# Kernel optimization log

Hardware: AMD Instinct MI355X
Metric: run time of the kernel (lower is better)

Reference implementation:

```python
import jax, jax.numpy as jnp
import numpy as np


def setup_inputs() -> dict:
    key = jax.random.key(0)
    k1, k2, k3 = jax.random.split(key, 3)
    B, H, S, D = 4, 16, 2048, 64
    return {
        "key": jax.random.normal(k1, (B, H, S, D), dtype=jnp.float32),
        "value": jax.random.normal(k2, (B, H, S, D), dtype=jnp.float32),
        "query": jax.random.normal(k3, (B, H, S, D), dtype=jnp.float32),
        # causal mask: True = attend, matches torch masked_fill_(~mask, -inf)
        "mask": jnp.tril(jnp.ones((S, S), dtype=jnp.bool_)),
    }


def reference(key, value, query, mask):
    # scores[b,h,q,k] = query . key^T  (mask applied before scaling as in the
    # source; -inf survives the divide so this equals standard masked attn)
    d = key.shape[-1]
    scores = jnp.einsum("bhqd,bhkd->bhqk", query, key)
    scores = jnp.where(mask, scores, -jnp.inf)
    scores = scores / jnp.sqrt(jnp.asarray(d, dtype=scores.dtype))
    attn = jax.nn.softmax(scores, axis=-1)
    # dropout omitted for a deterministic reference (eval mode)
    return jnp.einsum("bhqk,bhkd->bhqd", attn, value)
```

## Files before the change

### kernel.cpp

```cpp
#include <hip/hip_runtime.h>
#include <hip/hip_bf16.h>

typedef __attribute__((ext_vector_type(4))) float  f32x4;
typedef __attribute__((ext_vector_type(16))) float f32x16;
typedef __attribute__((ext_vector_type(8))) short  bf16x8v;
typedef __attribute__((ext_vector_type(4))) short  bf16x4v;

__device__ __forceinline__ unsigned short f2bf(float x) {
  __bf16 h = (__bf16)x;
  return __builtin_bit_cast(unsigned short, h);
}
__device__ __forceinline__ unsigned pk2(float lo, float hi2) {
  return (unsigned)f2bf(lo) | ((unsigned)f2bf(hi2) << 16);
}

constexpr int S  = 2048;
constexpr int D  = 64;
constexpr int BQ = 256;
constexpr int BK = 64;
#define KSCALE 0.18033688011112042f
#define DTHR   40.0f

__global__ __launch_bounds__(512, 4) void attn_fwd(
    const float* __restrict__ Kg, const float* __restrict__ Vg,
    const float* __restrict__ Qg, float* __restrict__ Og) {
  __shared__ unsigned short Kl[BK * D];
  __shared__ unsigned short Vt[D * BK];

  const int tid  = threadIdx.x;
  const int lane = tid & 63;
  const int w    = tid >> 6;
  const int l31  = lane & 31;
  const int hi   = lane >> 5;

  const int idx = (int)blockIdx.x;
  const int bh  = idx >> 3;
  const int qb  = (idx < 256) ? (7 - (idx & 7)) : (idx & 7);
  const int q0  = qb * BQ;

  const size_t base = (size_t)bh * S * D;
  const float* Kp = Kg + base;
  const float* Vp = Vg + base;
  const float* Qp = Qg + base;
  float*       Op = Og + base;

  const int qrow = q0 + w * 32 + l31;

  const int  st  = tid & 255;
  const bool isK = tid < 256;
  const int  krow = st >> 2, kcol0 = 16 * (st & 3);
  const int  kby0 = kcol0 * 2, kswz = (krow & 7) << 4;
  const int  vk0 = 4 * (st >> 4), vd0 = 4 * (st & 15);

  f32x4 pf0, pf1, pf2, pf3;

  auto LOAD = [&](int kt) {
    if (isK) {
      const float* p = Kp + (size_t)(kt * BK + krow) * D + kcol0;
      pf0 = *(const f32x4*)(p);      pf1 = *(const f32x4*)(p + 4);
      pf2 = *(const f32x4*)(p + 8);  pf3 = *(const f32x4*)(p + 12);
    } else {
      const float* p = Vp + (size_t)(kt * BK + vk0) * D + vd0;
      pf0 = *(const f32x4*)(p);          pf1 = *(const f32x4*)(p + D);
      pf2 = *(const f32x4*)(p + 2 * D);  pf3 = *(const f32x4*)(p + 3 * D);
    }
  };
  auto WRITE = [&]() {
    if (isK) {
      bf16x8v c0, c1;
      c0[0] = f2bf(pf0[0]); c0[1] = f2bf(pf0[1]); c0[2] = f2bf(pf0[2]); c0[3] = f2bf(pf0[3]);
      c0[4] = f2bf(pf1[0]); c0[5] = f2bf(pf1[1]); c0[6] = f2bf(pf1[2]); c0[7] = f2bf(pf1[3]);
      c1[0] = f2bf(pf2[0]); c1[1] = f2bf(pf2[1]); c1[2] = f2bf(pf2[2]); c1[3] = f2bf(pf2[3]);
      c1[4] = f2bf(pf3[0]); c1[5] = f2bf(pf3[1]); c1[6] = f2bf(pf3[2]); c1[7] = f2bf(pf3[3]);
      *(bf16x8v*)((char*)Kl + krow * 128 + ((kby0)      ^ kswz)) = c0;
      *(bf16x8v*)((char*)Kl + krow * 128 + ((kby0 + 16) ^ kswz)) = c1;
    } else {
#pragma unroll
      for (int j = 0; j < 4; ++j) {
        const int d = vd0 + j;
        bf16x4v tb;
        tb[0] = f2bf(pf0[j]); tb[1] = f2bf(pf1[j]);
        tb[2] = f2bf(pf2[j]); tb[3] = f2bf(pf3[j]);
        *(bf16x4v*)((char*)Vt + d * 128 + ((vk0 * 2) ^ ((d & 7) << 4))) = tb;
      }
    }
  };

  bf16x8v qf[4];
#pragma unroll
  for (int c = 0; c < 4; ++c) {
    const float* src = Qp + (size_t)qrow * D + c * 16 + hi * 8;
    f32x4 a = *(const f32x4*)src;
    f32x4 b = *(const f32x4*)(src + 4);
    bf16x8v f;
    f[0] = f2bf(a[0]); f[1] = f2bf(a[1]); f[2] = f2bf(a[2]); f[3] = f2bf(a[3]);
    f[4] = f2bf(b[0]); f[5] = f2bf(b[1]); f[6] = f2bf(b[2]); f[7] = f2bf(b[3]);
    qf[c] = f;
  }

  f32x16 acc0, acc1;
#pragma unroll
  for (int i = 0; i < 16; ++i) { acc0[i] = 0.f; acc1[i] = 0.f; }
  float mr = -INFINITY, lsum = 0.f;

  const int ktmax   = 4 * qb + 3;
  const int wave_dt = (q0 + 32 * w) >> 6;

  LOAD(0);

  for (int kt = 0; kt <= ktmax; ++kt) {
    __syncthreads();
    WRITE();
    if (kt < ktmax) LOAD(kt + 1);
    __syncthreads();

    if (kt <= wave_dt) {
      const int swz = (l31 & 7) << 4;

      f32x16 s0, s1;
#pragma unroll
      for (int i = 0; i < 16; ++i) { s0[i] = 0.f; s1[i] = 0.f; }
      __builtin_amdgcn_s_setprio(1);
#pragma unroll
      for (int c = 0; c < 4; ++c) {
        const int kb = c * 32 + hi * 16;
        bf16x8v ka0 = *(const bf16x8v*)((char*)Kl + l31 * 128 + (kb ^ swz));
        s0 = __builtin_amdgcn_mfma_f32_32x32x16_bf16(ka0, qf[c], s0, 0, 0, 0);
        bf16x8v ka1 = *(const bf16x8v*)((char*)Kl + (32 + l31) * 128 + (kb ^ swz));
        s1 = __builtin_amdgcn_mfma_f32_32x32x16_bf16(ka1, qf[c], s1, 0, 0, 0);
      }
      __builtin_amdgcn_s_setprio(0);

      if (kt == wave_dt) {
#pragma unroll
        for (int r = 0; r < 16; ++r) {
          const int crow = (r & 3) + 8 * (r >> 2) + 4 * hi;
          const int key0 = kt * BK + crow;
          if (key0      > qrow) s0[r] = -INFINITY;
          if (key0 + 32 > qrow) s1[r] = -INFINITY;
        }
      }

      float a0 = fmaxf(s0[0], s1[0]), a1 = fmaxf(s0[1], s1[1]);
      float a2 = fmaxf(s0[2], s1[2]), a3 = fmaxf(s0[3], s1[3]);
#pragma unroll
      for (int r = 4; r < 16; r += 4) {
        a0 = fmaxf(a0, fmaxf(s0[r],     s1[r]));
        a1 = fmaxf(a1, fmaxf(s0[r + 1], s1[r + 1]));
        a2 = fmaxf(a2, fmaxf(s0[r + 2], s1[r + 2]));
        a3 = fmaxf(a3, fmaxf(s0[r + 3], s1[r + 3]));
      }
      float mx = fmaxf(fmaxf(a0, a1), fmaxf(a2, a3));
      mx = fmaxf(mx, __shfl_xor(mx, 32));

      if (!__all(mx <= mr + DTHR)) {
        const float mnew = fmaxf(mr, mx);
        const float corr = __builtin_amdgcn_exp2f((mr - mnew) * KSCALE);
        mr = mnew;
        lsum *= corr;
#pragma unroll
        for (int i = 0; i < 16; ++i) { acc0[i] *= corr; acc1[i] *= corr; }
      }
      const float nb = mr * KSCALE;
#pragma unroll
      for (int r = 0; r < 16; ++r) {
        s0[r] = __builtin_amdgcn_exp2f(__builtin_fmaf(s0[r], KSCALE, -nb));
        s1[r] = __builtin_amdgcn_exp2f(__builtin_fmaf(s1[r], KSCALE, -nb));
      }
      float u0 = s0[0] + s1[0], u1 = s0[1] + s1[1];
      float u2 = s0[2] + s1[2], u3 = s0[3] + s1[3];
#pragma unroll
      for (int r = 4; r < 16; r += 4) {
        u0 += s0[r]     + s1[r];
        u1 += s0[r + 1] + s1[r + 1];
        u2 += s0[r + 2] + s1[r + 2];
        u3 += s0[r + 3] + s1[r + 3];
      }
      float ps = (u0 + u1) + (u2 + u3);
      ps += __shfl_xor(ps, 32);
      lsum += ps;

#pragma unroll
      for (int c = 0; c < 4; ++c) {
        const int rb = (c & 1) * 8;
        float p0, p1, p2, p3, p4, p5, p6, p7;
        if (c & 2) {
          p0 = s1[rb+0]; p1 = s1[rb+1]; p2 = s1[rb+2]; p3 = s1[rb+3];
          p4 = s1[rb+4]; p5 = s1[rb+5]; p6 = s1[rb+6]; p7 = s1[rb+7];
        } else {
          p0 = s0[rb+0]; p1 = s0[rb+1]; p2 = s0[rb+2]; p3 = s0[rb+3];
          p4 = s0[rb+4]; p5 = s0[rb+5]; p6 = s0[rb+6]; p7 = s0[rb+7];
        }
        const unsigned a0u = pk2(p0, p1), a1u = pk2(p2, p3);
        const unsigned b0u = pk2(p4, p5), b1u = pk2(p6, p7);
        const unsigned oa0 = (unsigned)__shfl_xor((int)a0u, 32);
        const unsigned oa1 = (unsigned)__shfl_xor((int)a1u, 32);
        const unsigned ob0 = (unsigned)__shfl_xor((int)b0u, 32);
        const unsigned ob1 = (unsigned)__shfl_xor((int)b1u, 32);
        union { unsigned u4[4]; bf16x8v v; } pw;
        pw.u4[0] = hi ? ob0 : a0u;
        pw.u4[1] = hi ? ob1 : a1u;
        pw.u4[2] = hi ? b0u : oa0;
        pw.u4[3] = hi ? b1u : oa1;
        const int kb = c * 32 + hi * 16;
        bf16x8v v0 = *(const bf16x8v*)((char*)Vt + l31 * 128 + (kb ^ swz));
        bf16x8v v1 = *(const bf16x8v*)((char*)Vt + (32 + l31) * 128 + (kb ^ swz));
        __builtin_amdgcn_s_setprio(1);
        acc0 = __builtin_amdgcn_mfma_f32_32x32x16_bf16(v0, pw.v, acc0, 0, 0, 0);
        acc1 = __builtin_amdgcn_mfma_f32_32x32x16_bf16(v1, pw.v, acc1, 0, 0, 0);
        __builtin_amdgcn_s_setprio(0);
      }
    }
  }

  const float inv = 1.0f / lsum;
#pragma unroll
  for (int mq = 0; mq < 4; ++mq) {
    const int dbase = 8 * mq + 4 * hi;
    f32x4 o0, o1;
#pragma unroll
    for (int i = 0; i < 4; ++i) {
      o0[i] = acc0[4 * mq + i] * inv;
      o1[i] = acc1[4 * mq + i] * inv;
    }
    *(f32x4*)(Op + (size_t)qrow * D + dbase)      = o0;
    *(f32x4*)(Op + (size_t)qrow * D + 32 + dbase) = o1;
  }
}

extern "C" void kernel_launch(void* const* d_in, const int* in_sizes, int n_in,
                              void* d_out, int out_size, void* d_ws, size_t ws_size,
                              hipStream_t stream) {
  const float* Kg = (const float*)d_in[0];
  const float* Vg = (const float*)d_in[1];
  const float* Qg = (const float*)d_in[2];
  float* Og = (float*)d_out;

  const int BH = 4 * 16;
  dim3 grid(BH * (S / BQ));
  dim3 block(512);
  attn_fwd<<<grid, block, 0, stream>>>(Kg, Vg, Qg, Og);
}
```

Before: 240.3 us.

## Halve query tile to 128 rows with 256-thread blocks and interleaved scheduling

Shrinks the query block from 256 to 128 rows, running 4 waves per block instead of 8, which doubles the grid to 1024 blocks. Each staging thread now loads twice as much K/V per tile. The block-to-tile mapping is reordered so batch-heads sit in the low bits and long causal tiles are scheduled first. The aim is better load balance across CUs and less intra-block wave imbalance from causal skipping, at the cost of loading each K/V tile twice as often overall.

```diff
diff --git a/kernel.cpp b/kernel.cpp
--- a/kernel.cpp
+++ b/kernel.cpp
@@ -16,12 +16,12 @@
 
 constexpr int S  = 2048;
 constexpr int D  = 64;
-constexpr int BQ = 256;
+constexpr int BQ = 128;
 constexpr int BK = 64;
 #define KSCALE 0.18033688011112042f
 #define DTHR   40.0f
 
-__global__ __launch_bounds__(512, 4) void attn_fwd(
+__global__ __launch_bounds__(256, 4) void attn_fwd(
     const float* __restrict__ Kg, const float* __restrict__ Vg,
     const float* __restrict__ Qg, float* __restrict__ Og) {
   __shared__ unsigned short Kl[BK * D];
@@ -34,9 +34,14 @@
   const int hi   = lane >> 5;
 
   const int idx = (int)blockIdx.x;
-  const int bh  = idx >> 3;
-  const int qb  = (idx < 256) ? (7 - (idx & 7)) : (idx & 7);
-  const int q0  = qb * BQ;
+  const int bh  = idx & 63;
+  const int g   = idx >> 6;
+  int qb;
+  if      (g < 4)  qb = 15 - 2 * g;
+  else if (g < 8)  qb = 22 - 2 * g;
+  else if (g < 12) qb = 2 * g - 15;
+  else             qb = 2 * g - 24;
+  const int q0 = qb * BQ;
 
   const size_t base = (size_t)bh * S * D;
   const float* Kp = Kg + base;
@@ -46,41 +51,48 @@
 
   const int qrow = q0 + w * 32 + l31;
 
-  const int  st  = tid & 255;
-  const bool isK = tid < 256;
-  const int  krow = st >> 2, kcol0 = 16 * (st & 3);
-  const int  kby0 = kcol0 * 2, kswz = (krow & 7) << 4;
-  const int  vk0 = 4 * (st >> 4), vd0 = 4 * (st & 15);
-
-  f32x4 pf0, pf1, pf2, pf3;
+  const int  st  = tid & 127;
+  const bool isK = tid < 128;
+  const int  krow = st >> 1, kcol0 = 32 * (st & 1);
+  const int  kswz = (krow & 7) << 4;
+  const int  vk0 = 4 * (st >> 3), vd0 = 8 * (st & 7);
+
+  f32x4 pf[8];
 
   auto LOAD = [&](int kt) {
     if (isK) {
       const float* p = Kp + (size_t)(kt * BK + krow) * D + kcol0;
-      pf0 = *(const f32x4*)(p);      pf1 = *(const f32x4*)(p + 4);
-      pf2 = *(const f32x4*)(p + 8);  pf3 = *(const f32x4*)(p + 12);
+#pragma unroll
+      for (int i = 0; i < 8; ++i) pf[i] = *(const f32x4*)(p + 4 * i);
     } else {
       const float* p = Vp + (size_t)(kt * BK + vk0) * D + vd0;
-      pf0 = *(const f32x4*)(p);          pf1 = *(const f32x4*)(p + D);
-      pf2 = *(const f32x4*)(p + 2 * D);  pf3 = *(const f32x4*)(p + 3 * D);
+#pragma unroll
+      for (int r = 0; r < 4; ++r) {
+        pf[2 * r]     = *(const f32x4*)(p + r * D);
+        pf[2 * r + 1] = *(const f32x4*)(p + r * D + 4);
+      }
     }
   };
   auto WRITE = [&]() {
     if (isK) {
-      bf16x8v c0, c1;
-      c0[0] = f2bf(pf0[0]); c0[1] = f2bf(pf0[1]); c0[2] = f2bf(pf0[2]); c0[3] = f2bf(pf0[3]);
-      c0[4] = f2bf(pf1[0]); c0[5] = f2bf(pf1[1]); c0[6] = f2bf(pf1[2]); c0[7] = f2bf(pf1[3]);
-      c1[0] = f2bf(pf2[0]); c1[1] = f2bf(pf2[1]); c1[2] = f2bf(pf2[2]); c1[3] = f2bf(pf2[3]);
-      c1[4] = f2bf(pf3[0]); c1[5] = f2bf(pf3[1]); c1[6] = f2bf(pf3[2]); c1[7] = f2bf(pf3[3]);
-      *(bf16x8v*)((char*)Kl + krow * 128 + ((kby0)      ^ kswz)) = c0;
-      *(bf16x8v*)((char*)Kl + krow * 128 + ((kby0 + 16) ^ kswz)) = c1;
+#pragma unroll
+      for (int i = 0; i < 4; ++i) {
+        bf16x8v cc;
+        cc[0] = f2bf(pf[2*i][0]);   cc[1] = f2bf(pf[2*i][1]);
+        cc[2] = f2bf(pf[2*i][2]);   cc[3] = f2bf(pf[2*i][3]);
+        cc[4] = f2bf(pf[2*i+1][0]); cc[5] = f2bf(pf[2*i+1][1]);
+        cc[6] = f2bf(pf[2*i+1][2]); cc[7] = f2bf(pf[2*i+1][3]);
+        *(bf16x8v*)((char*)Kl + krow * 128 + ((kcol0 * 2 + 16 * i) ^ kswz)) = cc;
+      }
     } else {
 #pragma unroll
-      for (int j = 0; j < 4; ++j) {
+      for (int j = 0; j < 8; ++j) {
         const int d = vd0 + j;
         bf16x4v tb;
-        tb[0] = f2bf(pf0[j]); tb[1] = f2bf(pf1[j]);
-        tb[2] = f2bf(pf2[j]); tb[3] = f2bf(pf3[j]);
+        tb[0] = f2bf(pf[0 + (j >> 2)][j & 3]);
+        tb[1] = f2bf(pf[2 + (j >> 2)][j & 3]);
+        tb[2] = f2bf(pf[4 + (j >> 2)][j & 3]);
+        tb[3] = f2bf(pf[6 + (j >> 2)][j & 3]);
         *(bf16x4v*)((char*)Vt + d * 128 + ((vk0 * 2) ^ ((d & 7) << 4))) = tb;
       }
     }
@@ -103,7 +115,7 @@
   for (int i = 0; i < 16; ++i) { acc0[i] = 0.f; acc1[i] = 0.f; }
   float mr = -INFINITY, lsum = 0.f;
 
-  const int ktmax   = 4 * qb + 3;
+  const int ktmax   = 2 * qb + 1;
   const int wave_dt = (q0 + 32 * w) >> 6;
 
   LOAD(0);
@@ -238,6 +250,6 @@
 
   const int BH = 4 * 16;
   dim3 grid(BH * (S / BQ));
-  dim3 block(512);
+  dim3 block(256);
   attn_fwd<<<grid, block, 0, stream>>>(Kg, Vg, Qg, Og);
 }
```

Result: slower. 327.8 us (+36.4%).
